# Optimization experiments

Measured on AMD Instinct MI355X. Metric: run time of the kernel, lower is better.

## Reference

```python
import jax, jax.numpy as jnp
import numpy as np

B, S, E, H, DH = 4, 2048, 2048, 16, 256  # DH = mlp hidden (d_hid)
HD = E // H  # per-head dim = 128
EPS = 1e-5

def _ln(x, w, b):
    m = jnp.mean(x, axis=-1, keepdims=True)
    v = jnp.mean(jnp.square(x - m), axis=-1, keepdims=True)
    return (x - m) * jax.lax.rsqrt(v + EPS) * w + b

def setup_inputs() -> dict:
    key = jax.random.key(0)
    ks = jax.random.split(key, 10)
    s = 0.02
    return {
        "x": jax.random.normal(ks[0], (B, S, E), jnp.float32),
        "attention_mask": jax.random.randint(ks[1], (B, S), 0, 2, jnp.int32),
        "ln1_w": jnp.ones((E,), jnp.float32),
        "ln1_b": jnp.zeros((E,), jnp.float32),
        "in_proj_w": jax.random.normal(ks[2], (3 * E, E), jnp.float32) * s,
        "in_proj_b": jnp.zeros((3 * E,), jnp.float32),
        "out_proj_w": jax.random.normal(ks[3], (E, E), jnp.float32) * s,
        "out_proj_b": jnp.zeros((E,), jnp.float32),
        "ln2_w": jnp.ones((E,), jnp.float32),
        "ln2_b": jnp.zeros((E,), jnp.float32),
        "mlp_w1": jax.random.normal(ks[4], (DH, E), jnp.float32) * s,
        "mlp_b1": jnp.zeros((DH,), jnp.float32),
        "mlp_w2": jax.random.normal(ks[5], (E, DH), jnp.float32) * s,
        "mlp_b2": jnp.zeros((E,), jnp.float32),
    }

def reference(x, attention_mask, ln1_w, ln1_b, in_proj_w, in_proj_b,
              out_proj_w, out_proj_b, ln2_w, ln2_b, mlp_w1, mlp_b1, mlp_w2, mlp_b2):
    h = _ln(x, ln1_w, ln1_b)
    qkv = h @ in_proj_w.T + in_proj_b  # [B,S,3E]
    q, k, v = jnp.split(qkv, 3, axis=-1)
    q = q.reshape(B, S, H, HD).transpose(0, 2, 1, 3) / jnp.sqrt(jnp.float32(HD))
    k = k.reshape(B, S, H, HD).transpose(0, 2, 1, 3)
    v = v.reshape(B, S, H, HD).transpose(0, 2, 1, 3)
    scores = jnp.einsum("bhqd,bhkd->bhqk", q, k)
    # Faithful to source: FLOAT attn_mask of +1.0 on strictly-upper triangle (additive),
    # NOT -inf; key_padding_mask positions do get -inf.
    causal_add = jnp.triu(jnp.ones((S, S), jnp.float32), k=1)
    scores = scores + causal_add
    pad = (attention_mask == 0)  # True = padded key
    scores = jnp.where(pad[:, None, None, :], jnp.float32(-jnp.inf), scores)
    attn = jax.nn.softmax(scores, axis=-1)
    ctx = jnp.einsum("bhqk,bhkd->bhqd", attn, v)
    ctx = ctx.transpose(0, 2, 1, 3).reshape(B, S, E)
    x = x + ctx @ out_proj_w.T + out_proj_b
    h2 = _ln(x, ln2_w, ln2_b)
    mlp = jax.nn.relu(h2 @ mlp_w1.T + mlp_b1) @ mlp_w2.T + mlp_b2
    return x + mlp
```

## Files before the change

### kernel.cpp

```cpp
#include <hip/hip_runtime.h>

typedef __attribute__((ext_vector_type(8))) short short8;
typedef __attribute__((ext_vector_type(4))) float f32x4;
typedef __attribute__((ext_vector_type(16))) float f32x16;

typedef __attribute__((address_space(1))) const void gas1_t;
typedef __attribute__((address_space(3))) void las3_t;
#define GLL16(g, l) __builtin_amdgcn_global_load_lds((gas1_t*)(g), (las3_t*)(l), 16, 0, 0)

__device__ inline unsigned short f2bf(float f) {
  union { float f; unsigned int u; } v; v.f = f;
  unsigned int r = v.u + 0x7FFFu + ((v.u >> 16) & 1u);
  return (unsigned short)(r >> 16);
}

__device__ inline float exp2_fast(float x) {
  float r; asm("v_exp_f32 %0, %1" : "=v"(r) : "v"(x)); return r;
}

__device__ inline void vmwait(int n) {
  if (n == 6)      asm volatile("s_waitcnt vmcnt(6)" ::: "memory");
  else             asm volatile("s_waitcnt vmcnt(0)" ::: "memory");
}

__global__ __launch_bounds__(256) void ln_kernel(const float* __restrict__ x,
                                                 const float* __restrict__ w,
                                                 const float* __restrict__ bia,
                                                 unsigned short* __restrict__ out) {
  const int row = blockIdx.x;
  const int tid = threadIdx.x;
  const float* xr = x + (size_t)row * 2048;
  float4 a = *(const float4*)(xr + tid * 8);
  float4 b = *(const float4*)(xr + tid * 8 + 4);
  float s  = a.x + a.y + a.z + a.w + b.x + b.y + b.z + b.w;
  float s2 = a.x*a.x + a.y*a.y + a.z*a.z + a.w*a.w + b.x*b.x + b.y*b.y + b.z*b.z + b.w*b.w;
  #pragma unroll
  for (int off = 1; off < 64; off <<= 1) {
    s  += __shfl_xor(s, off);
    s2 += __shfl_xor(s2, off);
  }
  __shared__ float red[8];
  if ((tid & 63) == 0) { red[tid >> 6] = s; red[4 + (tid >> 6)] = s2; }
  __syncthreads();
  s  = red[0] + red[1] + red[2] + red[3];
  s2 = red[4] + red[5] + red[6] + red[7];
  const float mean = s * (1.f / 2048.f);
  const float var  = s2 * (1.f / 2048.f) - mean * mean;
  const float rstd = rsqrtf(var + 1e-5f);
  float4 wa = *(const float4*)(w + tid * 8), wb = *(const float4*)(w + tid * 8 + 4);
  float4 ba = *(const float4*)(bia + tid * 8), bb = *(const float4*)(bia + tid * 8 + 4);
  short8 o;
  o[0] = (short)f2bf((a.x - mean) * rstd * wa.x + ba.x);
  o[1] = (short)f2bf((a.y - mean) * rstd * wa.y + ba.y);
  o[2] = (short)f2bf((a.z - mean) * rstd * wa.z + ba.z);
  o[3] = (short)f2bf((a.w - mean) * rstd * wa.w + ba.w);
  o[4] = (short)f2bf((b.x - mean) * rstd * wb.x + bb.x);
  o[5] = (short)f2bf((b.y - mean) * rstd * wb.y + bb.y);
  o[6] = (short)f2bf((b.z - mean) * rstd * wb.z + bb.z);
  o[7] = (short)f2bf((b.w - mean) * rstd * wb.w + bb.w);
  *(short8*)(out + (size_t)row * 2048 + tid * 8) = o;
}

__global__ __launch_bounds__(256) void conv_kernel(const float* __restrict__ in,
                                                   unsigned short* __restrict__ out, int n) {
  size_t idx = ((size_t)blockIdx.x * 256 + threadIdx.x) * 8;
  if (idx >= (size_t)n) return;
  float4 a = *(const float4*)(in + idx);
  float4 b = *(const float4*)(in + idx + 4);
  short8 o;
  o[0] = (short)f2bf(a.x); o[1] = (short)f2bf(a.y);
  o[2] = (short)f2bf(a.z); o[3] = (short)f2bf(a.w);
  o[4] = (short)f2bf(b.x); o[5] = (short)f2bf(b.y);
  o[6] = (short)f2bf(b.z); o[7] = (short)f2bf(b.w);
  *(short8*)(out + idx) = o;
}

template <int MODE>
__global__ __launch_bounds__(256) void gemm_bt(const unsigned short* __restrict__ A,
                                               const unsigned short* __restrict__ Bw,
                                               const float* __restrict__ bias,
                                               const float* __restrict__ res,
                                               void* __restrict__ outp,
                                               void* __restrict__ outp2,
                                               int M, int N, int K) {
  __shared__ unsigned short As[128 * 64];
  __shared__ unsigned short Bs[128 * 64];
  const int tid = threadIdx.x;
  const int l = tid & 63, wv = tid >> 6;
  const int l15 = l & 15, l4 = l >> 4;
  const int wr = wv >> 1, wc = wv & 1;
  const int nx = gridDim.x;
  const int nwg = nx * gridDim.y;
  const int bidlin = blockIdx.y * nx + blockIdx.x;
  const int cpx = nwg >> 3;
  const int swz = (bidlin & 7) * cpx + (bidlin >> 3);
  const int m0 = (swz / nx) * 128, n0 = (swz % nx) * 128;

  f32x4 acc[4][4] = {};
  for (int k0 = 0; k0 < K; k0 += 64) {
    __syncthreads();
    #pragma unroll
    for (int i = 0; i < 4; ++i) {
      int e = i * 2048 + tid * 8;
      int r = e >> 6;
      int c = (e ^ ((r & 7) << 3)) & 63;
      GLL16(A + (size_t)(m0 + r) * K + k0 + c, As + e);
      GLL16(Bw + (size_t)(n0 + r) * K + k0 + c, Bs + e);
    }
    __syncthreads();
    #pragma unroll
    for (int kk = 0; kk < 64; kk += 32) {
      short8 af[4], bfr[4];
      #pragma unroll
      for (int m = 0; m < 4; ++m) {
        int r = wr * 64 + m * 16 + l15;
        int byt = (r * 128 + (kk + l4 * 8) * 2) ^ ((r & 7) << 4);
        af[m] = *(const short8*)((const char*)As + byt);
      }
      #pragma unroll
      for (int n = 0; n < 4; ++n) {
        int r = wc * 64 + n * 16 + l15;
        int byt = (r * 128 + (kk + l4 * 8) * 2) ^ ((r & 7) << 4);
        bfr[n] = *(const short8*)((const char*)Bs + byt);
      }
      #pragma unroll
      for (int m = 0; m < 4; ++m)
        #pragma unroll
        for (int n = 0; n < 4; ++n)
          acc[m][n] = __builtin_amdgcn_mfma_f32_16x16x32_bf16(af[m], bfr[n], acc[m][n], 0, 0, 0);
    }
  }
  #pragma unroll
  for (int m = 0; m < 4; ++m) {
    #pragma unroll
    for (int n = 0; n < 4; ++n) {
      #pragma unroll
      for (int r = 0; r < 4; ++r) {
        int row = m0 + wr * 64 + m * 16 + l4 * 4 + r;
        int col = n0 + wc * 64 + n * 16 + l15;
        float v = acc[m][n][r] + bias[col];
        if (MODE == 1) {
          ((unsigned short*)outp)[(size_t)row * N + col] = f2bf(v > 0.f ? v : 0.f);
        } else {
          ((float*)outp)[(size_t)row * N + col] = res[(size_t)row * N + col] + v;
        }
      }
    }
  }
}

template <int MODE>
__global__ __launch_bounds__(512, 2) void gemm8(const unsigned short* __restrict__ A,
                                                const unsigned short* __restrict__ Bw,
                                                const float* __restrict__ bias,
                                                const float* __restrict__ res,
                                                void* __restrict__ outp,
                                                void* __restrict__ outp2,
                                                int M, int N, int K) {
  __shared__ char LA[2][2][16384];
  __shared__ char LB[2][2][16384];
  const int tid = threadIdx.x;
  const int l = tid & 63, wv = tid >> 6;
  const int l15 = l & 15, l4 = l >> 4;
  const int wr = wv >> 2, wc = wv & 3;
  const int wch = wc >> 1, wcl = wc & 1;
  const int nx = gridDim.x;
  const int nwg = nx * gridDim.y;
  const int bidlin = blockIdx.y * nx + blockIdx.x;
  const int cpx = nwg >> 3;
  const int swz = (bidlin & 7) * cpx + (bidlin >> 3);
  const int m0 = (swz / nx) * 256, n0 = (swz % nx) * 256;

  const int srow = tid >> 3;
  const int scol = ((tid & 7) ^ (srow & 7)) * 8;

#define STG_A(x, h) { const unsigned short* bp = A + (size_t)(m0 + (h) * 128) * K + (x) * 64; \
    GLL16(bp + (size_t)srow * K + scol, &LA[(x) & 1][h][tid * 16]); \
    GLL16(bp + (size_t)(srow + 64) * K + scol, &LA[(x) & 1][h][8192 + tid * 16]); }
#define STG_B(x, h) { const unsigned short* bp = Bw + (size_t)(n0 + (h) * 128) * K + (x) * 64; \
    GLL16(bp + (size_t)srow * K + scol, &LB[(x) & 1][h][tid * 16]); \
    GLL16(bp + (size_t)(srow + 64) * K + scol, &LB[(x) & 1][h][8192 + tid * 16]); }

#define FOFF(r, kh) ((r) * 128 + (((((kh) * 4 + l4)) ^ ((r) & 7)) << 4))

  f32x4 acc[8][4] = {};
  const int NT = K >> 6;

  STG_A(0, 0); STG_A(0, 1); STG_B(0, 0); STG_B(0, 1);
  STG_B(1, 0); STG_B(1, 1); STG_A(1, 0);
  vmwait(6);
  __builtin_amdgcn_s_barrier();

#define MFMAK(mh, kh) \
    __builtin_amdgcn_s_setprio(1); \
    _Pragma("unroll") for (int f = 0; f < 4; ++f) \
      _Pragma("unroll") for (int n = 0; n < 4; ++n) \
        acc[(mh) * 4 + f][n] = __builtin_amdgcn_mfma_f32_16x16x32_bf16( \
            af[kh][f], bfr[kh][n], acc[(mh) * 4 + f][n], 0, 0, 0); \
    __builtin_amdgcn_s_setprio(0);

  for (int t = 0; t < NT; ++t) {
    const char* Ab = LA[t & 1][wr];
    const char* Bb = LB[t & 1][wch];
    short8 af[2][4], bfr[2][4];
    #pragma unroll
    for (int f = 0; f < 4; ++f) {
      bfr[0][f] = *(const short8*)(Bb + FOFF(wcl * 64 + f * 16 + l15, 0));
      af[0][f]  = *(const short8*)(Ab + FOFF(f * 16 + l15, 0));
    }
    __builtin_amdgcn_sched_barrier(0);
    #pragma unroll
    for (int f = 0; f < 4; ++f) {
      bfr[1][f] = *(const short8*)(Bb + FOFF(wcl * 64 + f * 16 + l15, 1));
      af[1][f]  = *(const short8*)(Ab + FOFF(f * 16 + l15, 1));
    }
    if (t + 1 < NT) STG_A(t + 1, 1);
    __builtin_amdgcn_s_barrier();
    asm volatile("s_waitcnt lgkmcnt(8)" ::: "memory");
    __builtin_amdgcn_sched_barrier(0);
    MFMAK(0, 0);
    asm volatile("s_waitcnt lgkmcnt(0)" ::: "memory");
    __builtin_amdgcn_sched_barrier(0);
    MFMAK(0, 1);
    __builtin_amdgcn_s_barrier();
    #pragma unroll
    for (int f = 0; f < 4; ++f)
      af[0][f] = *(const short8*)(Ab + FOFF(64 + f * 16 + l15, 0));
    __builtin_amdgcn_sched_barrier(0);
    #pragma unroll
    for (int f = 0; f < 4; ++f)
      af[1][f] = *(const short8*)(Ab + FOFF(64 + f * 16 + l15, 1));
    if (t + 2 < NT) { STG_B(t + 2, 0); STG_B(t + 2, 1); STG_A(t + 2, 0); }
    __builtin_amdgcn_s_barrier();
    asm volatile("s_waitcnt lgkmcnt(4)" ::: "memory");
    __builtin_amdgcn_sched_barrier(0);
    MFMAK(1, 0);
    asm volatile("s_waitcnt lgkmcnt(0)" ::: "memory");
    __builtin_amdgcn_sched_barrier(0);
    MFMAK(1, 1);
    vmwait(t >= NT - 2 ? 0 : 6);
    __builtin_amdgcn_s_barrier();
  }
#undef MFMAK
#undef FOFF
#undef STG_A
#undef STG_B

  #pragma unroll
  for (int mf = 0; mf < 8; ++mf) {
    #pragma unroll
    for (int nf = 0; nf < 4; ++nf) {
      #pragma unroll
      for (int r = 0; r < 4; ++r) {
        int row = m0 + wr * 128 + mf * 16 + l4 * 4 + r;
        int col = n0 + wc * 64 + nf * 16 + l15;
        float v = acc[mf][nf][r] + bias[col];
        if (MODE == 0) {
          unsigned short val = f2bf(v);
          if (col < 4096) ((unsigned short*)outp)[(size_t)row * 4096 + col] = val;
          else            ((unsigned short*)outp2)[(size_t)row * 2048 + col - 4096] = val;
        } else {
          ((float*)outp)[(size_t)row * N + col] = res[(size_t)row * N + col] + v;
        }
      }
    }
  }
}

__global__ __launch_bounds__(256) void vtrans_kernel(const unsigned short* __restrict__ v,
                                                     unsigned short* __restrict__ vT) {
  __shared__ unsigned short T[128 * 128];
  const int t0 = blockIdx.x * 128;
  const int b = blockIdx.y >> 4, h = blockIdx.y & 15;
  const int tid = threadIdx.x;
  const int tl = tid >> 4, l16 = tid & 15, c8 = l16 * 8;
  #pragma unroll
  for (int i = 0; i < 8; ++i) {
    int t = tl + i * 16;
    short8 val = *(const short8*)(v + (size_t)(b * 2048 + t0 + t) * 2048 + h * 128 + c8);
    *(short8*)((char*)T + ((t * 256 + c8 * 2) ^ ((t & 7) << 4))) = val;
  }
  __syncthreads();
  #pragma unroll
  for (int i = 0; i < 8; ++i) {
    int d = tl + i * 16;
    unsigned short* orow = vT + ((size_t)(b * 16 + h) * 128 + d) * 2048 + t0;
    #pragma unroll
    for (int j = 0; j < 8; ++j) {
      int t = l16 + 16 * j;
      orow[t] = *(const unsigned short*)((const char*)T + ((t * 256 + d * 2) ^ ((t & 7) << 4)));
    }
  }
}

__global__ __launch_bounds__(256) void attn_kernel(const unsigned short* __restrict__ qk,
                                                   const unsigned short* __restrict__ vT,
                                                   const int* __restrict__ amask,
                                                   unsigned short* __restrict__ ctx) {
  __shared__ unsigned short Ks[2][4096];
  __shared__ unsigned short Vs[2][4096];

  const int lin = blockIdx.y * 16 + blockIdx.x;
  const int swzb = (lin & 7) * 128 + (lin >> 3);
  const int qt = swzb & 15, bh = swzb >> 4;
  const int b = bh >> 4, h = bh & 15;
  const int tid = threadIdx.x;
  const int wv = tid >> 6, l = tid & 63;
  const int l31 = l & 31, hi = l >> 5;
  const int q0w = qt * 128 + wv * 32;
  const float SC2 = 0.08838834764831845f * 1.4426950408889634f;
  const float L2E = 1.4426950408889634f;
  const float MF  = 10.0f;

  int kinv[2], vinv[2];
  #pragma unroll
  for (int c = 0; c < 2; ++c) {
    int e = c * 2048 + tid * 8;
    int key = e >> 7, d0 = e & 127;
    kinv[c] = key * 4096 + 2048 + h * 128 + (d0 ^ ((key & 7) << 3));
    int d = e >> 5, kchunk = ((e >> 3) & 3) ^ ((d & 6) >> 1);
    vinv[c] = d * 2048 + kchunk * 8;
  }
  const unsigned short* kb0 = qk + (size_t)(b * 2048) * 4096;
  const unsigned short* vb0 = vT + (size_t)(b * 16 + h) * (128 * 2048);
  const int* mrow = amask + b * 2048;

  short8 qf[8];
  {
    const unsigned short* qp = qk + (size_t)(b * 2048 + q0w + l31) * 4096 + h * 128 + hi * 8;
    #pragma unroll
    for (int c = 0; c < 8; ++c) qf[c] = *(const short8*)(qp + c * 16);
  }

  short8 vones;
  #pragma unroll
  for (int j = 0; j < 8; ++j) vones[j] = (short)0x3F80;

  f32x16 o[4] = {};
  f32x16 ol = {};

  #pragma unroll
  for (int c = 0; c < 2; ++c) {
    GLL16(kb0 + kinv[c], &Ks[0][c * 2048 + tid * 8]);
    GLL16(vb0 + vinv[c], &Vs[0][c * 2048 + tid * 8]);
  }
  __syncthreads();

  for (int kt = 0; kt < 2048; kt += 32) {
    const int cur = (kt >> 5) & 1;
    if (kt + 32 < 2048) {
      #pragma unroll
      for (int c = 0; c < 2; ++c) {
        GLL16(kb0 + (size_t)(kt + 32) * 4096 + kinv[c], &Ks[cur ^ 1][c * 2048 + tid * 8]);
        GLL16(vb0 + (kt + 32) + vinv[c], &Vs[cur ^ 1][c * 2048 + tid * 8]);
      }
    }
    const unsigned bm = (unsigned)__ballot((l < 32) && (mrow[kt + l31] == 0));
    const unsigned bmh = bm >> (4 * hi);

    f32x16 sacc = {};
    __builtin_amdgcn_s_setprio(1);
    #pragma unroll
    for (int c = 0; c < 8; ++c) {
      short8 kf = *(const short8*)((const char*)Ks[cur] +
                   ((l31 * 256 + c * 32 + hi * 16) ^ ((l31 & 7) << 4)));
      sacc = __builtin_amdgcn_mfma_f32_32x32x16_bf16(kf, qf[c], sacc, 0, 0, 0);
    }
    __builtin_amdgcn_s_setprio(0);

    const int Dq = q0w + l31 - kt - 4 * hi;
    float p[16];
    if (kt > q0w + 31) {
      #pragma unroll
      for (int i = 0; i < 16; ++i) p[i] = sacc[i] * SC2 + (L2E - MF);
    } else if (kt + 31 <= q0w) {
      #pragma unroll
      for (int i = 0; i < 16; ++i) p[i] = sacc[i] * SC2 - MF;
    } else {
      #pragma unroll
      for (int i = 0; i < 16; ++i) {
        const int ci = (i & 3) + 8 * (i >> 2);
        p[i] = sacc[i] * SC2 + ((ci > Dq) ? (L2E - MF) : -MF);
      }
    }
    #pragma unroll
    for (int i = 0; i < 16; ++i) {
      const int ci = (i & 3) + 8 * (i >> 2);
      if ((bmh >> ci) & 1) p[i] = -1e30f;
    }
    #pragma unroll
    for (int i = 0; i < 16; ++i) p[i] = exp2_fast(p[i]);

#define CVTPK(dst, a, bsrc) asm("v_cvt_pk_bf16_f32 %0, %1, %2" : "=v"(dst) : "v"(a), "v"(bsrc))
#define PLSWAP(fst, snd) asm("v_permlane32_swap_b32 %0, %1" : "+v"(fst), "+v"(snd))
    unsigned x, x2, y, y2, u, u2, v, v2;
    CVTPK(x,  p[0],  p[1]);  CVTPK(x2, p[2],  p[3]);
    CVTPK(y,  p[4],  p[5]);  CVTPK(y2, p[6],  p[7]);
    CVTPK(u,  p[8],  p[9]);  CVTPK(u2, p[10], p[11]);
    CVTPK(v,  p[12], p[13]); CVTPK(v2, p[14], p[15]);
    PLSWAP(x, y);  PLSWAP(x2, y2);
    PLSWAP(u, v);  PLSWAP(u2, v2);
    union { unsigned w[4]; short8 s8; } P0, P1;
    P0.w[0] = x; P0.w[1] = x2; P0.w[2] = y; P0.w[3] = y2;
    P1.w[0] = u; P1.w[1] = u2; P1.w[2] = v; P1.w[3] = v2;
    short8 pa0 = P0.s8, pa1 = P1.s8;
#undef CVTPK
#undef PLSWAP

    __builtin_amdgcn_s_setprio(1);
    #pragma unroll
    for (int g = 0; g < 4; ++g) {
      int d = g * 32 + l31;
      int swzd = (d & 6) << 3;
      short8 vf0 = *(const short8*)((const char*)Vs[cur] + ((d * 64 + hi * 16) ^ swzd));
      o[g] = __builtin_amdgcn_mfma_f32_32x32x16_bf16(pa0, vf0, o[g], 0, 0, 0);
      short8 vf1 = *(const short8*)((const char*)Vs[cur] + ((d * 64 + 32 + hi * 16) ^ swzd));
      o[g] = __builtin_amdgcn_mfma_f32_32x32x16_bf16(pa1, vf1, o[g], 0, 0, 0);
    }
    ol = __builtin_amdgcn_mfma_f32_32x32x16_bf16(pa0, vones, ol, 0, 0, 0);
    ol = __builtin_amdgcn_mfma_f32_32x32x16_bf16(pa1, vones, ol, 0, 0, 0);
    __builtin_amdgcn_s_setprio(0);

    __syncthreads();
  }

  float inv[16];
  #pragma unroll
  for (int i = 0; i < 16; ++i) inv[i] = 1.0f / ol[i];
  #pragma unroll
  for (int g = 0; g < 4; ++g) {
    #pragma unroll
    for (int i = 0; i < 16; ++i) {
      int q = q0w + (i & 3) + 8 * (i >> 2) + 4 * hi;
      ctx[(size_t)(b * 2048 + q) * 2048 + h * 128 + g * 32 + l31] = f2bf(o[g][i] * inv[i]);
    }
  }
}

extern "C" void kernel_launch(void* const* d_in, const int* in_sizes, int n_in,
                              void* d_out, int out_size, void* d_ws, size_t ws_size,
                              hipStream_t stream) {
  (void)in_sizes; (void)n_in; (void)out_size; (void)ws_size;
  const float* x    = (const float*)d_in[0];
  const int*   am   = (const int*)d_in[1];
  const float* ln1w = (const float*)d_in[2];
  const float* ln1b = (const float*)d_in[3];
  const float* win  = (const float*)d_in[4];
  const float* bin  = (const float*)d_in[5];
  const float* wout = (const float*)d_in[6];
  const float* bout = (const float*)d_in[7];
  const float* ln2w = (const float*)d_in[8];
  const float* ln2b = (const float*)d_in[9];
  const float* w1   = (const float*)d_in[10];
  const float* b1   = (const float*)d_in[11];
  const float* w2   = (const float*)d_in[12];
  const float* b2   = (const float*)d_in[13];
  float* out = (float*)d_out;

  char* ws = (char*)d_ws;
  unsigned short* hbuf = (unsigned short*)ws;
  unsigned short* vTb  = (unsigned short*)ws;
  unsigned short* qkb  = (unsigned short*)(ws + (size_t)32 * 1048576);
  unsigned short* h2b  = (unsigned short*)(ws + (size_t)32 * 1048576);
  unsigned short* midb = (unsigned short*)(ws + (size_t)64 * 1048576);
  unsigned short* vbuf = (unsigned short*)(ws + (size_t)96 * 1048576);
  unsigned short* ctxb = (unsigned short*)(ws + (size_t)96 * 1048576);
  unsigned short* wbuf = (unsigned short*)(ws + (size_t)128 * 1048576);

  ln_kernel<<<dim3(8192), dim3(256), 0, stream>>>(x, ln1w, ln1b, hbuf);
  conv_kernel<<<dim3(6144), dim3(256), 0, stream>>>(win, wbuf, 12582912);
  gemm8<0><<<dim3(24, 32), dim3(512), 0, stream>>>(hbuf, wbuf, bin, (const float*)nullptr,
                                                   (void*)qkb, (void*)vbuf, 8192, 6144, 2048);
  vtrans_kernel<<<dim3(16, 64), dim3(256), 0, stream>>>(vbuf, vTb);
  attn_kernel<<<dim3(16, 64), dim3(256), 0, stream>>>(qkb, vTb, am, ctxb);
  conv_kernel<<<dim3(2048), dim3(256), 0, stream>>>(wout, wbuf, 4194304);
  gemm8<2><<<dim3(8, 32), dim3(512), 0, stream>>>(ctxb, wbuf, bout, x,
                                                  (void*)out, nullptr, 8192, 2048, 2048);
  ln_kernel<<<dim3(8192), dim3(256), 0, stream>>>(out, ln2w, ln2b, h2b);
  conv_kernel<<<dim3(256), dim3(256), 0, stream>>>(w1, wbuf, 524288);
  gemm_bt<1><<<dim3(2, 64), dim3(256), 0, stream>>>(h2b, wbuf, b1, (const float*)nullptr,
                                                    (void*)midb, nullptr, 8192, 256, 2048);
  conv_kernel<<<dim3(256), dim3(256), 0, stream>>>(w2, wbuf, 524288);
  gemm8<2><<<dim3(8, 32), dim3(512), 0, stream>>>(midb, wbuf, b2, out,
                                                  (void*)out, nullptr, 8192, 2048, 256);
}
```

Baseline: 607.9 us.

## Fuse V transpose into V projection GEMM epilogue via swapped MFMA operands

Splits the QKV GEMM into a Q/K GEMM and a separate V GEMM (MODE 3). The V GEMM swaps the MFMA operands so that each lane holds consecutive tokens, then writes V directly in transposed per-head layout. This removes the standalone vtrans kernel and its extra read and write of V. In exchange there is an extra kernel launch, a smaller grid per GEMM, and strided 2-byte stores in the transposed epilogue.

```diff
diff --git a/kernel.cpp b/kernel.cpp
--- a/kernel.cpp
+++ b/kernel.cpp
@@ -155,7 +155,6 @@
                                                 const float* __restrict__ bias,
                                                 const float* __restrict__ res,
                                                 void* __restrict__ outp,
-                                                void* __restrict__ outp2,
                                                 int M, int N, int K) {
   __shared__ char LA[2][2][16384];
   __shared__ char LB[2][2][16384];
@@ -194,9 +193,14 @@
 #define MFMAK(mh, kh) \
     __builtin_amdgcn_s_setprio(1); \
     _Pragma("unroll") for (int f = 0; f < 4; ++f) \
-      _Pragma("unroll") for (int n = 0; n < 4; ++n) \
-        acc[(mh) * 4 + f][n] = __builtin_amdgcn_mfma_f32_16x16x32_bf16( \
-            af[kh][f], bfr[kh][n], acc[(mh) * 4 + f][n], 0, 0, 0); \
+      _Pragma("unroll") for (int n = 0; n < 4; ++n) { \
+        if (MODE == 3) \
+          acc[(mh) * 4 + f][n] = __builtin_amdgcn_mfma_f32_16x16x32_bf16( \
+              bfr[kh][n], af[kh][f], acc[(mh) * 4 + f][n], 0, 0, 0); \
+        else \
+          acc[(mh) * 4 + f][n] = __builtin_amdgcn_mfma_f32_16x16x32_bf16( \
+              af[kh][f], bfr[kh][n], acc[(mh) * 4 + f][n], 0, 0, 0); \
+      } \
     __builtin_amdgcn_s_setprio(0);
 
   for (int t = 0; t < NT; ++t) {
@@ -252,43 +256,25 @@
     for (int nf = 0; nf < 4; ++nf) {
       #pragma unroll
       for (int r = 0; r < 4; ++r) {
-        int row = m0 + wr * 128 + mf * 16 + l4 * 4 + r;
-        int col = n0 + wc * 64 + nf * 16 + l15;
-        float v = acc[mf][nf][r] + bias[col];
-        if (MODE == 0) {
-          unsigned short val = f2bf(v);
-          if (col < 4096) ((unsigned short*)outp)[(size_t)row * 4096 + col] = val;
-          else            ((unsigned short*)outp2)[(size_t)row * 2048 + col - 4096] = val;
+        if (MODE == 3) {
+          int vcol = n0 + wc * 64 + nf * 16 + l4 * 4 + r;
+          int token = m0 + wr * 128 + mf * 16 + l15;
+          float v = acc[mf][nf][r] + bias[vcol];
+          int hh = vcol >> 7, d = vcol & 127;
+          int bb = token >> 11;
+          ((unsigned short*)outp)[((size_t)(bb * 16 + hh) * 128 + d) * 2048 +
+                                  (token & 2047)] = f2bf(v);
         } else {
-          ((float*)outp)[(size_t)row * N + col] = res[(size_t)row * N + col] + v;
+          int row = m0 + wr * 128 + mf * 16 + l4 * 4 + r;
+          int col = n0 + wc * 64 + nf * 16 + l15;
+          float v = acc[mf][nf][r] + bias[col];
+          if (MODE == 0) {
+            ((unsigned short*)outp)[(size_t)row * 4096 + col] = f2bf(v);
+          } else {
+            ((float*)outp)[(size_t)row * N + col] = res[(size_t)row * N + col] + v;
+          }
         }
       }
-    }
-  }
-}
-
-__global__ __launch_bounds__(256) void vtrans_kernel(const unsigned short* __restrict__ v,
-                                                     unsigned short* __restrict__ vT) {
-  __shared__ unsigned short T[128 * 128];
-  const int t0 = blockIdx.x * 128;
-  const int b = blockIdx.y >> 4, h = blockIdx.y & 15;
-  const int tid = threadIdx.x;
-  const int tl = tid >> 4, l16 = tid & 15, c8 = l16 * 8;
-  #pragma unroll
-  for (int i = 0; i < 8; ++i) {
-    int t = tl + i * 16;
-    short8 val = *(const short8*)(v + (size_t)(b * 2048 + t0 + t) * 2048 + h * 128 + c8);
-    *(short8*)((char*)T + ((t * 256 + c8 * 2) ^ ((t & 7) << 4))) = val;
-  }
-  __syncthreads();
-  #pragma unroll
-  for (int i = 0; i < 8; ++i) {
-    int d = tl + i * 16;
-    unsigned short* orow = vT + ((size_t)(b * 16 + h) * 128 + d) * 2048 + t0;
-    #pragma unroll
-    for (int j = 0; j < 8; ++j) {
-      int t = l16 + 16 * j;
-      orow[t] = *(const unsigned short*)((const char*)T + ((t * 256 + d * 2) ^ ((t & 7) << 4)));
     }
   }
 }
@@ -459,28 +445,29 @@
 
   char* ws = (char*)d_ws;
   unsigned short* hbuf = (unsigned short*)ws;
-  unsigned short* vTb  = (unsigned short*)ws;
+  unsigned short* ctxb = (unsigned short*)ws;
   unsigned short* qkb  = (unsigned short*)(ws + (size_t)32 * 1048576);
   unsigned short* h2b  = (unsigned short*)(ws + (size_t)32 * 1048576);
   unsigned short* midb = (unsigned short*)(ws + (size_t)64 * 1048576);
-  unsigned short* vbuf = (unsigned short*)(ws + (size_t)96 * 1048576);
-  unsigned short* ctxb = (unsigned short*)(ws + (size_t)96 * 1048576);
+  unsigned short* vTb  = (unsigned short*)(ws + (size_t)96 * 1048576);
   unsigned short* wbuf = (unsigned short*)(ws + (size_t)128 * 1048576);
 
   ln_kernel<<<dim3(8192), dim3(256), 0, stream>>>(x, ln1w, ln1b, hbuf);
   conv_kernel<<<dim3(6144), dim3(256), 0, stream>>>(win, wbuf, 12582912);
-  gemm8<0><<<dim3(24, 32), dim3(512), 0, stream>>>(hbuf, wbuf, bin, (const float*)nullptr,
-                                                   (void*)qkb, (void*)vbuf, 8192, 6144, 2048);
-  vtrans_kernel<<<dim3(16, 64), dim3(256), 0, stream>>>(vbuf, vTb);
+  gemm8<0><<<dim3(16, 32), dim3(512), 0, stream>>>(hbuf, wbuf, bin, (const float*)nullptr,
+                                                   (void*)qkb, 8192, 4096, 2048);
+  gemm8<3><<<dim3(8, 32), dim3(512), 0, stream>>>(hbuf, wbuf + (size_t)4096 * 2048,
+                                                  bin + 4096, (const float*)nullptr,
+                                                  (void*)vTb, 8192, 2048, 2048);
   attn_kernel<<<dim3(16, 64), dim3(256), 0, stream>>>(qkb, vTb, am, ctxb);
   conv_kernel<<<dim3(2048), dim3(256), 0, stream>>>(wout, wbuf, 4194304);
   gemm8<2><<<dim3(8, 32), dim3(512), 0, stream>>>(ctxb, wbuf, bout, x,
-                                                  (void*)out, nullptr, 8192, 2048, 2048);
+                                                  (void*)out, 8192, 2048, 2048);
   ln_kernel<<<dim3(8192), dim3(256), 0, stream>>>(out, ln2w, ln2b, h2b);
   conv_kernel<<<dim3(256), dim3(256), 0, stream>>>(w1, wbuf, 524288);
   gemm_bt<1><<<dim3(2, 64), dim3(256), 0, stream>>>(h2b, wbuf, b1, (const float*)nullptr,
                                                     (void*)midb, nullptr, 8192, 256, 2048);
   conv_kernel<<<dim3(256), dim3(256), 0, stream>>>(w2, wbuf, 524288);
   gemm8<2><<<dim3(8, 32), dim3(512), 0, stream>>>(midb, wbuf, b2, out,
-                                                  (void*)out, nullptr, 8192, 2048, 256);
-}
+                                                  (void*)out, 8192, 2048, 256);
+}
```

Measured after the change: 592.4 us. 1.03x faster.
